# Optimization experiments

Hardware: AMD Instinct MI355X
Metric: run time of the kernel (lower is better)

Reference implementation:

```python
import jax, jax.numpy as jnp
import numpy as np

N_QUBITS = 4
N_LAYERS = 3
SHORT_W = 2048
LONG_W = 8192
BATCH = 2048


def _conv1d(x, w, b, pad):
    # x: [B, Cin, L], w: [Cout, Cin, K]
    y = jax.lax.conv_general_dilated(x, w, window_strides=(1,), padding=[(pad, pad)],
                                     dimension_numbers=("NCH", "OIH", "NCH"))
    return y + b[None, :, None]


def _ry_mat(t):
    c, s = jnp.cos(t / 2), jnp.sin(t / 2)
    return jnp.stack([jnp.stack([c, -s]), jnp.stack([s, c])]).astype(jnp.complex64)


def _rz_mat(a):
    return jnp.diag(jnp.stack([jnp.exp(-0.5j * a), jnp.exp(0.5j * a)])).astype(jnp.complex64)


def _rot_mat(phi, theta, omega):
    # PennyLane Rot(phi, theta, omega) = RZ(omega) @ RY(theta) @ RZ(phi)
    return _rz_mat(omega) @ _ry_mat(theta) @ _rz_mat(phi)


def _apply_1q(state, U, wire):
    state = jnp.tensordot(U, state, axes=((1,), (wire,)))
    return jnp.moveaxis(state, 0, wire)


def _apply_cnot(state, c, t):
    s0 = jax.lax.index_in_dim(state, 0, axis=c, keepdims=True)
    s1 = jax.lax.index_in_dim(state, 1, axis=c, keepdims=True)
    s1 = jnp.flip(s1, axis=t)
    return jnp.concatenate([s0, s1], axis=c)


def _circuit(x, w):
    # x: [4] real features, w: [3, 4, 3] StronglyEntanglingLayers weights
    state = jnp.zeros((2,) * N_QUBITS, jnp.complex64).at[(0,) * N_QUBITS].set(1.0)
    for i in range(N_QUBITS):
        state = _apply_1q(state, _ry_mat(jnp.pi * x[i]), i)
    for l in range(N_LAYERS):
        r = (l % (N_QUBITS - 1)) + 1  # default PennyLane ranges: 1,2,3
        for i in range(N_QUBITS):
            state = _apply_1q(state, _rot_mat(w[l, i, 0], w[l, i, 1], w[l, i, 2]), i)
        for i in range(N_QUBITS):
            state = _apply_cnot(state, i, (i + r) % N_QUBITS)
    probs = jnp.abs(state) ** 2
    zs = []
    for i in range(N_QUBITS):
        p = probs.sum(axis=tuple(a for a in range(N_QUBITS) if a != i))
        zs.append(p[0] - p[1])  # <PauliZ_i>
    return jnp.stack(zs)


def setup_inputs() -> dict:
    key = jax.random.key(0)
    ks = jax.random.split(key, 13)
    d = {}
    d["xs"] = jax.random.normal(ks[0], (BATCH, 1, SHORT_W), jnp.float32)
    d["xl"] = jax.random.normal(ks[1], (BATCH, 1, LONG_W), jnp.float32)
    d["cs_conv_w"] = jax.random.normal(ks[2], (8, 1, 3), jnp.float32) * 0.3
    d["cs_conv_b"] = jax.random.normal(ks[3], (8,), jnp.float32) * 0.1
    d["cs_lin_w"] = jax.random.normal(ks[4], (2, 8 * SHORT_W), jnp.float32) * (1.0 / np.sqrt(8 * SHORT_W))
    d["cs_lin_b"] = jax.random.normal(ks[5], (2,), jnp.float32) * 0.1
    d["cl_conv_w"] = jax.random.normal(ks[6], (8, 1, 5), jnp.float32) * 0.3
    d["cl_conv_b"] = jax.random.normal(ks[7], (8,), jnp.float32) * 0.1
    d["cl_lin_w"] = jax.random.normal(ks[8], (2, 8 * LONG_W // 2), jnp.float32) * (1.0 / np.sqrt(8 * LONG_W // 2))
    d["cl_lin_b"] = jax.random.normal(ks[9], (2,), jnp.float32) * 0.1
    d["rw"] = jax.random.normal(ks[10], (N_LAYERS, N_QUBITS, 3), jnp.float32)
    d["fc_w"] = jax.random.normal(ks[11], (1, N_QUBITS), jnp.float32) * 0.5
    d["fc_b"] = jax.random.normal(ks[12], (1,), jnp.float32) * 0.1
    return d


def reference(xs, xl, cs_conv_w, cs_conv_b, cs_lin_w, cs_lin_b,
              cl_conv_w, cl_conv_b, cl_lin_w, cl_lin_b, rw, fc_w, fc_b):
    B = xs.shape[0]
    # short branch: conv(k=3,p=1) -> relu -> flatten -> linear
    hs = jax.nn.relu(_conv1d(xs, cs_conv_w, cs_conv_b, 1)).reshape(B, -1)
    fs = hs @ cs_lin_w.T + cs_lin_b  # [B, 2]
    # long branch: conv(k=5,p=2) -> relu -> maxpool(2) -> flatten -> linear
    hl = jax.nn.relu(_conv1d(xl, cl_conv_w, cl_conv_b, 2))
    hl = hl.reshape(B, 8, LONG_W // 2, 2).max(axis=-1).reshape(B, -1)
    fl = hl @ cl_lin_w.T + cl_lin_b  # [B, 2]
    f = jnp.concatenate([fs, fl], axis=1)  # [B, 4]
    # original detaches features before the quantum circuit
    f = jax.lax.stop_gradient(f)
    rw_c = jax.lax.stop_gradient(rw)
    qo = jax.vmap(lambda x: _circuit(x, rw_c))(f).astype(jnp.float32)  # [B, 4]
    return qo @ fc_w.T + fc_b  # [B, 1]
```

## Files before the change

### kernel.cpp

```cpp
#include <hip/hip_runtime.h>
#include <math.h>

namespace {
constexpr int kB  = 2048;
constexpr int kSW = 2048;
constexpr int kLW = 8192;
constexpr int kLP = kLW / 2;
constexpr int kROWS = 4;
constexpr int kLBLKS = (kB / kROWS) * 2;
constexpr int kSBLKS = (kB / kROWS) * 2;
}

__device__ __forceinline__ void long_half(
    int blk, int h, const float* __restrict__ xl, const float* __restrict__ cw,
    const float* __restrict__ cb, const float* __restrict__ lw,
    float* __restrict__ part) {
  __shared__ float red[kROWS][2][4];
  const int tid = threadIdx.x;
  const int b0 = blk * kROWS;

  float wgt[8][5], bias[8];
#pragma unroll
  for (int c = 0; c < 8; ++c) {
#pragma unroll
    for (int k = 0; k < 5; ++k) wgt[c][k] = cw[c * 5 + k];
    bias[c] = cb[c];
  }

  float acc[kROWS][2];
#pragma unroll
  for (int r = 0; r < kROWS; ++r) { acc[r][0] = 0.f; acc[r][1] = 0.f; }

  for (int ch = 0; ch < 2; ++ch) {
    const int p0 = h * 2048 + ch * 1024 + tid * 4;
    const int s  = 2 * p0;

    float w[kROWS][12];
#pragma unroll
    for (int r = 0; r < kROWS; ++r) {
      const float* x = xl + (size_t)(b0 + r) * kLW;
      float2 hm = (p0 > 0) ? *reinterpret_cast<const float2*>(x + s - 2)
                           : make_float2(0.f, 0.f);
      float4 f0 = *reinterpret_cast<const float4*>(x + s);
      float4 f1 = *reinterpret_cast<const float4*>(x + s + 4);
      float2 f2 = (s + 8 < kLW) ? *reinterpret_cast<const float2*>(x + s + 8)
                                : make_float2(0.f, 0.f);
      w[r][0] = hm.x; w[r][1] = hm.y;
      w[r][2] = f0.x; w[r][3] = f0.y; w[r][4] = f0.z; w[r][5] = f0.w;
      w[r][6] = f1.x; w[r][7] = f1.y; w[r][8] = f1.z; w[r][9] = f1.w;
      w[r][10] = f2.x; w[r][11] = f2.y;
    }
    float4 la4[8], lb4[8];
#pragma unroll
    for (int c = 0; c < 8; ++c) {
      la4[c] = *reinterpret_cast<const float4*>(lw + (size_t)c * kLP + p0);
      lb4[c] = *reinterpret_cast<const float4*>(lw + (size_t)(8 + c) * kLP + p0);
    }

#pragma unroll
    for (int c = 0; c < 8; ++c) {
      const float la[4] = {la4[c].x, la4[c].y, la4[c].z, la4[c].w};
      const float lbv[4] = {lb4[c].x, lb4[c].y, lb4[c].z, lb4[c].w};
#pragma unroll
      for (int r = 0; r < kROWS; ++r) {
#pragma unroll
        for (int u = 0; u < 4; ++u) {
          float v0 = fmaf(wgt[c][0], w[r][2 * u + 0],
                     fmaf(wgt[c][1], w[r][2 * u + 1],
                     fmaf(wgt[c][2], w[r][2 * u + 2],
                     fmaf(wgt[c][3], w[r][2 * u + 3],
                     fmaf(wgt[c][4], w[r][2 * u + 4], bias[c])))));
          float v1 = fmaf(wgt[c][0], w[r][2 * u + 1],
                     fmaf(wgt[c][1], w[r][2 * u + 2],
                     fmaf(wgt[c][2], w[r][2 * u + 3],
                     fmaf(wgt[c][3], w[r][2 * u + 4],
                     fmaf(wgt[c][4], w[r][2 * u + 5], bias[c])))));
          const float m = fmaxf(fmaxf(v0, v1), 0.f);
          acc[r][0] = fmaf(m, la[u], acc[r][0]);
          acc[r][1] = fmaf(m, lbv[u], acc[r][1]);
        }
      }
    }
  }

#pragma unroll
  for (int r = 0; r < kROWS; ++r)
#pragma unroll
    for (int o = 0; o < 2; ++o) {
      float a = acc[r][o];
#pragma unroll
      for (int off = 32; off > 0; off >>= 1) a += __shfl_down(a, off);
      if ((tid & 63) == 0) red[r][o][tid >> 6] = a;
    }
  __syncthreads();
  if (tid < kROWS * 2) {
    const int r = tid >> 1, o = tid & 1;
    part[(size_t)h * kB * 4 + (size_t)(b0 + r) * 4 + 2 + o] =
        red[r][o][0] + red[r][o][1] + red[r][o][2] + red[r][o][3];
  }
}

__device__ __forceinline__ void short_half(
    int blk, int h, const float* __restrict__ xs, const float* __restrict__ cw,
    const float* __restrict__ cb, const float* __restrict__ lw,
    float* __restrict__ part) {
  __shared__ float red[kROWS][2][4];
  const int tid = threadIdx.x;
  const int b0 = blk * kROWS;

  float wgt[8][3], bias[8];
#pragma unroll
  for (int c = 0; c < 8; ++c) {
#pragma unroll
    for (int k = 0; k < 3; ++k) wgt[c][k] = cw[c * 3 + k];
    bias[c] = cb[c];
  }

  float acc[kROWS][2];
#pragma unroll
  for (int r = 0; r < kROWS; ++r) { acc[r][0] = 0.f; acc[r][1] = 0.f; }

  {
    const int p0 = h * 1024 + tid * 4;

    float w[kROWS][6];
#pragma unroll
    for (int r = 0; r < kROWS; ++r) {
      const float* x = xs + (size_t)(b0 + r) * kSW;
      float xm = (p0 > 0) ? x[p0 - 1] : 0.f;
      float4 f0 = *reinterpret_cast<const float4*>(x + p0);
      float xp = (p0 + 4 < kSW) ? x[p0 + 4] : 0.f;
      w[r][0] = xm;
      w[r][1] = f0.x; w[r][2] = f0.y; w[r][3] = f0.z; w[r][4] = f0.w;
      w[r][5] = xp;
    }
    float4 la4[8], lb4[8];
#pragma unroll
    for (int c = 0; c < 8; ++c) {
      la4[c] = *reinterpret_cast<const float4*>(lw + (size_t)c * kSW + p0);
      lb4[c] = *reinterpret_cast<const float4*>(lw + (size_t)(8 + c) * kSW + p0);
    }

#pragma unroll
    for (int c = 0; c < 8; ++c) {
      const float la[4] = {la4[c].x, la4[c].y, la4[c].z, la4[c].w};
      const float lbv[4] = {lb4[c].x, lb4[c].y, lb4[c].z, lb4[c].w};
#pragma unroll
      for (int r = 0; r < kROWS; ++r) {
#pragma unroll
        for (int u = 0; u < 4; ++u) {
          float v = fmaf(wgt[c][0], w[r][u],
                    fmaf(wgt[c][1], w[r][u + 1],
                    fmaf(wgt[c][2], w[r][u + 2], bias[c])));
          const float m = fmaxf(v, 0.f);
          acc[r][0] = fmaf(m, la[u], acc[r][0]);
          acc[r][1] = fmaf(m, lbv[u], acc[r][1]);
        }
      }
    }
  }

#pragma unroll
  for (int r = 0; r < kROWS; ++r)
#pragma unroll
    for (int o = 0; o < 2; ++o) {
      float a = acc[r][o];
#pragma unroll
      for (int off = 32; off > 0; off >>= 1) a += __shfl_down(a, off);
      if ((tid & 63) == 0) red[r][o][tid >> 6] = a;
    }
  __syncthreads();
  if (tid < kROWS * 2) {
    const int r = tid >> 1, o = tid & 1;
    part[(size_t)h * kB * 4 + (size_t)(b0 + r) * 4 + o] =
        red[r][o][0] + red[r][o][1] + red[r][o][2] + red[r][o][3];
  }
}

__global__ __launch_bounds__(256, 3) void features_kernel(
    const float* __restrict__ xs, const float* __restrict__ cs_cw,
    const float* __restrict__ cs_cb, const float* __restrict__ cs_lw,
    const float* __restrict__ xl, const float* __restrict__ cl_cw,
    const float* __restrict__ cl_cb, const float* __restrict__ cl_lw,
    float* __restrict__ part) {
  const int bid = blockIdx.x;
  if (bid < kLBLKS)
    long_half(bid >> 1, bid & 1, xl, cl_cw, cl_cb, cl_lw, part);
  else {
    const int s = bid - kLBLKS;
    short_half(s >> 1, s & 1, xs, cs_cw, cs_cb, cs_lw, part);
  }
}

template <int MASK>
__device__ __forceinline__ void apply_1q(float (&ar)[16], float (&ai)[16],
                                         float u00r, float u00i, float u01r, float u01i,
                                         float u10r, float u10i, float u11r, float u11i) {
#pragma unroll
  for (int i = 0; i < 16; ++i) {
    if (!(i & MASK)) {
      const int j = i | MASK;
      const float a0r = ar[i], a0i = ai[i];
      const float a1r = ar[j], a1i = ai[j];
      ar[i] = u00r * a0r - u00i * a0i + u01r * a1r - u01i * a1i;
      ai[i] = u00r * a0i + u00i * a0r + u01r * a1i + u01i * a1r;
      ar[j] = u10r * a0r - u10i * a0i + u11r * a1r - u11i * a1i;
      ai[j] = u10r * a0i + u10i * a0r + u11r * a1i + u11i * a1r;
    }
  }
}

template <int MASK>
__device__ __forceinline__ void apply_ry(float (&ar)[16], float (&ai)[16], float half_t) {
  float s, c;
  sincosf(half_t, &s, &c);
  apply_1q<MASK>(ar, ai, c, 0.f, -s, 0.f, s, 0.f, c, 0.f);
}

template <int MASK>
__device__ __forceinline__ void apply_rot(float (&ar)[16], float (&ai)[16],
                                          float phi, float theta, float omega) {
  float st, ct; sincosf(0.5f * theta, &st, &ct);
  float sa, ca; sincosf(0.5f * (phi + omega), &sa, &ca);
  float sm, cm; sincosf(0.5f * (phi - omega), &sm, &cm);
  apply_1q<MASK>(ar, ai,
                 ct * ca, -ct * sa,
                 -st * cm, -st * sm,
                 st * cm, -st * sm,
                 ct * ca, ct * sa);
}

template <int MC, int MT>
__device__ __forceinline__ void apply_cnot(float (&ar)[16], float (&ai)[16]) {
#pragma unroll
  for (int i = 0; i < 16; ++i) {
    if ((i & MC) && !(i & MT)) {
      const int j = i | MT;
      float t;
      t = ar[i]; ar[i] = ar[j]; ar[j] = t;
      t = ai[i]; ai[i] = ai[j]; ai[j] = t;
    }
  }
}

__global__ __launch_bounds__(64) void quantum_kernel(
    const float* __restrict__ part, const float* __restrict__ cs_lb,
    const float* __restrict__ cl_lb, const float* __restrict__ rw,
    const float* __restrict__ fcw, const float* __restrict__ fcb,
    float* __restrict__ out) {
  const int b = blockIdx.x * 64 + threadIdx.x;
  if (b >= kB) return;

  const float f0 = part[(size_t)b * 4 + 0] + part[(size_t)kB * 4 + b * 4 + 0] + cs_lb[0];
  const float f1 = part[(size_t)b * 4 + 1] + part[(size_t)kB * 4 + b * 4 + 1] + cs_lb[1];
  const float f2 = part[(size_t)b * 4 + 2] + part[(size_t)kB * 4 + b * 4 + 2] + cl_lb[0];
  const float f3 = part[(size_t)b * 4 + 3] + part[(size_t)kB * 4 + b * 4 + 3] + cl_lb[1];

  float ar[16], ai[16];
#pragma unroll
  for (int i = 0; i < 16; ++i) { ar[i] = 0.f; ai[i] = 0.f; }
  ar[0] = 1.f;

  const float kHalfPi = 1.57079632679489662f;
  apply_ry<8>(ar, ai, kHalfPi * f0);
  apply_ry<4>(ar, ai, kHalfPi * f1);
  apply_ry<2>(ar, ai, kHalfPi * f2);
  apply_ry<1>(ar, ai, kHalfPi * f3);

  apply_rot<8>(ar, ai, rw[0], rw[1], rw[2]);
  apply_rot<4>(ar, ai, rw[3], rw[4], rw[5]);
  apply_rot<2>(ar, ai, rw[6], rw[7], rw[8]);
  apply_rot<1>(ar, ai, rw[9], rw[10], rw[11]);
  apply_cnot<8, 4>(ar, ai);
  apply_cnot<4, 2>(ar, ai);
  apply_cnot<2, 1>(ar, ai);
  apply_cnot<1, 8>(ar, ai);

  apply_rot<8>(ar, ai, rw[12], rw[13], rw[14]);
  apply_rot<4>(ar, ai, rw[15], rw[16], rw[17]);
  apply_rot<2>(ar, ai, rw[18], rw[19], rw[20]);
  apply_rot<1>(ar, ai, rw[21], rw[22], rw[23]);
  apply_cnot<8, 2>(ar, ai);
  apply_cnot<4, 1>(ar, ai);
  apply_cnot<2, 8>(ar, ai);
  apply_cnot<1, 4>(ar, ai);

  apply_rot<8>(ar, ai, rw[24], rw[25], rw[26]);
  apply_rot<4>(ar, ai, rw[27], rw[28], rw[29]);
  apply_rot<2>(ar, ai, rw[30], rw[31], rw[32]);
  apply_rot<1>(ar, ai, rw[33], rw[34], rw[35]);
  apply_cnot<8, 1>(ar, ai);
  apply_cnot<4, 8>(ar, ai);
  apply_cnot<2, 4>(ar, ai);
  apply_cnot<1, 2>(ar, ai);

  float z0 = 0.f, z1 = 0.f, z2 = 0.f, z3 = 0.f;
#pragma unroll
  for (int i = 0; i < 16; ++i) {
    const float p = ar[i] * ar[i] + ai[i] * ai[i];
    z0 += (i & 8) ? -p : p;
    z1 += (i & 4) ? -p : p;
    z2 += (i & 2) ? -p : p;
    z3 += (i & 1) ? -p : p;
  }
  out[b] = fcb[0] + z0 * fcw[0] + z1 * fcw[1] + z2 * fcw[2] + z3 * fcw[3];
}

extern "C" void kernel_launch(void* const* d_in, const int* in_sizes, int n_in,
                              void* d_out, int out_size, void* d_ws, size_t ws_size,
                              hipStream_t stream) {
  const float* xs     = (const float*)d_in[0];
  const float* xl     = (const float*)d_in[1];
  const float* cs_cw  = (const float*)d_in[2];
  const float* cs_cb  = (const float*)d_in[3];
  const float* cs_lw  = (const float*)d_in[4];
  const float* cs_lb  = (const float*)d_in[5];
  const float* cl_cw  = (const float*)d_in[6];
  const float* cl_cb  = (const float*)d_in[7];
  const float* cl_lw  = (const float*)d_in[8];
  const float* cl_lb  = (const float*)d_in[9];
  const float* rw     = (const float*)d_in[10];
  const float* fcw    = (const float*)d_in[11];
  const float* fcb    = (const float*)d_in[12];
  float* out  = (float*)d_out;
  float* part = (float*)d_ws;

  hipLaunchKernelGGL(features_kernel, dim3(kLBLKS + kSBLKS), dim3(256), 0, stream,
                     xs, cs_cw, cs_cb, cs_lw,
                     xl, cl_cw, cl_cb, cl_lw, part);
  hipLaunchKernelGGL(quantum_kernel, dim3(kB / 64), dim3(64), 0, stream,
                     part, cs_lb, cl_lb, rw, fcw, fcb, out);
}
```

Before: 46.52 us.

## Split long-branch work into quarters, interleave block types, pin operands in registers

Each long-branch block now covers one quarter of the pooled sequence instead of a half with an inner two-chunk loop. Long and short blocks are interleaved two-to-one in the grid so both kinds are spread evenly across CUs. Linear-weight and input values are loaded once up front and pinned in VGPRs with empty asm, and rows are processed in pairs to keep register pressure down. The partial-sum layout changes to separate short and long buffers, with the quantum kernel summing four long partials. This means more blocks and more partial writes, and the register pinning may hurt occupancy or scheduling.

```diff
diff --git a/kernel.cpp b/kernel.cpp
--- a/kernel.cpp
+++ b/kernel.cpp
@@ -7,14 +7,15 @@
 constexpr int kLW = 8192;
 constexpr int kLP = kLW / 2;
 constexpr int kROWS = 4;
-constexpr int kLBLKS = (kB / kROWS) * 2;
-constexpr int kSBLKS = (kB / kROWS) * 2;
-}
-
-__device__ __forceinline__ void long_half(
-    int blk, int h, const float* __restrict__ xl, const float* __restrict__ cw,
+constexpr int kNBLK = 3072;
+}
+
+__device__ __forceinline__ void pin(float& x) { asm volatile("" : "+v"(x)); }
+
+__device__ __forceinline__ void long_quarter(
+    int blk, int q, const float* __restrict__ xl, const float* __restrict__ cw,
     const float* __restrict__ cb, const float* __restrict__ lw,
-    float* __restrict__ part) {
+    float* __restrict__ partL) {
   __shared__ float red[kROWS][2][4];
   const int tid = threadIdx.x;
   const int b0 = blk * kROWS;
@@ -27,18 +28,32 @@
     bias[c] = cb[c];
   }
 
+  const int p0 = q * 1024 + tid * 4;
+  const int s  = 2 * p0;
+
+  float la[8][4], lbv[8][4];
+#pragma unroll
+  for (int c = 0; c < 8; ++c) {
+    float4 a4 = *reinterpret_cast<const float4*>(lw + (size_t)c * kLP + p0);
+    float4 b4 = *reinterpret_cast<const float4*>(lw + (size_t)(8 + c) * kLP + p0);
+    la[c][0] = a4.x; la[c][1] = a4.y; la[c][2] = a4.z; la[c][3] = a4.w;
+    lbv[c][0] = b4.x; lbv[c][1] = b4.y; lbv[c][2] = b4.z; lbv[c][3] = b4.w;
+  }
+#pragma unroll
+  for (int c = 0; c < 8; ++c)
+#pragma unroll
+    for (int u = 0; u < 4; ++u) { pin(la[c][u]); pin(lbv[c][u]); }
+
   float acc[kROWS][2];
 #pragma unroll
   for (int r = 0; r < kROWS; ++r) { acc[r][0] = 0.f; acc[r][1] = 0.f; }
 
-  for (int ch = 0; ch < 2; ++ch) {
-    const int p0 = h * 2048 + ch * 1024 + tid * 4;
-    const int s  = 2 * p0;
-
-    float w[kROWS][12];
-#pragma unroll
-    for (int r = 0; r < kROWS; ++r) {
-      const float* x = xl + (size_t)(b0 + r) * kLW;
+#pragma unroll
+  for (int g = 0; g < 2; ++g) {
+    float w[2][12];
+#pragma unroll
+    for (int r = 0; r < 2; ++r) {
+      const float* x = xl + (size_t)(b0 + g * 2 + r) * kLW;
       float2 hm = (p0 > 0) ? *reinterpret_cast<const float2*>(x + s - 2)
                            : make_float2(0.f, 0.f);
       float4 f0 = *reinterpret_cast<const float4*>(x + s);
@@ -50,19 +65,16 @@
       w[r][6] = f1.x; w[r][7] = f1.y; w[r][8] = f1.z; w[r][9] = f1.w;
       w[r][10] = f2.x; w[r][11] = f2.y;
     }
-    float4 la4[8], lb4[8];
+#pragma unroll
+    for (int r = 0; r < 2; ++r)
+#pragma unroll
+      for (int k = 0; k < 12; ++k) pin(w[r][k]);
+
 #pragma unroll
     for (int c = 0; c < 8; ++c) {
-      la4[c] = *reinterpret_cast<const float4*>(lw + (size_t)c * kLP + p0);
-      lb4[c] = *reinterpret_cast<const float4*>(lw + (size_t)(8 + c) * kLP + p0);
-    }
-
-#pragma unroll
-    for (int c = 0; c < 8; ++c) {
-      const float la[4] = {la4[c].x, la4[c].y, la4[c].z, la4[c].w};
-      const float lbv[4] = {lb4[c].x, lb4[c].y, lb4[c].z, lb4[c].w};
-#pragma unroll
-      for (int r = 0; r < kROWS; ++r) {
+#pragma unroll
+      for (int r = 0; r < 2; ++r) {
+        const int rr = g * 2 + r;
 #pragma unroll
         for (int u = 0; u < 4; ++u) {
           float v0 = fmaf(wgt[c][0], w[r][2 * u + 0],
@@ -76,8 +88,8 @@
                      fmaf(wgt[c][3], w[r][2 * u + 4],
                      fmaf(wgt[c][4], w[r][2 * u + 5], bias[c])))));
           const float m = fmaxf(fmaxf(v0, v1), 0.f);
-          acc[r][0] = fmaf(m, la[u], acc[r][0]);
-          acc[r][1] = fmaf(m, lbv[u], acc[r][1]);
+          acc[rr][0] = fmaf(m, la[c][u], acc[rr][0]);
+          acc[rr][1] = fmaf(m, lbv[c][u], acc[rr][1]);
         }
       }
     }
@@ -95,7 +107,7 @@
   __syncthreads();
   if (tid < kROWS * 2) {
     const int r = tid >> 1, o = tid & 1;
-    part[(size_t)h * kB * 4 + (size_t)(b0 + r) * 4 + 2 + o] =
+    partL[(size_t)q * kB * 2 + (size_t)(b0 + r) * 2 + o] =
         red[r][o][0] + red[r][o][1] + red[r][o][2] + red[r][o][3];
   }
 }
@@ -103,7 +115,7 @@
 __device__ __forceinline__ void short_half(
     int blk, int h, const float* __restrict__ xs, const float* __restrict__ cw,
     const float* __restrict__ cb, const float* __restrict__ lw,
-    float* __restrict__ part) {
+    float* __restrict__ partS) {
   __shared__ float red[kROWS][2][4];
   const int tid = threadIdx.x;
   const int b0 = blk * kROWS;
@@ -116,46 +128,53 @@
     bias[c] = cb[c];
   }
 
+  const int p0 = h * 1024 + tid * 4;
+
+  float la[8][4], lbv[8][4];
+#pragma unroll
+  for (int c = 0; c < 8; ++c) {
+    float4 a4 = *reinterpret_cast<const float4*>(lw + (size_t)c * kSW + p0);
+    float4 b4 = *reinterpret_cast<const float4*>(lw + (size_t)(8 + c) * kSW + p0);
+    la[c][0] = a4.x; la[c][1] = a4.y; la[c][2] = a4.z; la[c][3] = a4.w;
+    lbv[c][0] = b4.x; lbv[c][1] = b4.y; lbv[c][2] = b4.z; lbv[c][3] = b4.w;
+  }
+#pragma unroll
+  for (int c = 0; c < 8; ++c)
+#pragma unroll
+    for (int u = 0; u < 4; ++u) { pin(la[c][u]); pin(lbv[c][u]); }
+
+  float w[kROWS][6];
+#pragma unroll
+  for (int r = 0; r < kROWS; ++r) {
+    const float* x = xs + (size_t)(b0 + r) * kSW;
+    float xm = (p0 > 0) ? x[p0 - 1] : 0.f;
+    float4 f0 = *reinterpret_cast<const float4*>(x + p0);
+    float xp = (p0 + 4 < kSW) ? x[p0 + 4] : 0.f;
+    w[r][0] = xm;
+    w[r][1] = f0.x; w[r][2] = f0.y; w[r][3] = f0.z; w[r][4] = f0.w;
+    w[r][5] = xp;
+  }
+#pragma unroll
+  for (int r = 0; r < kROWS; ++r)
+#pragma unroll
+    for (int k = 0; k < 6; ++k) pin(w[r][k]);
+
   float acc[kROWS][2];
 #pragma unroll
   for (int r = 0; r < kROWS; ++r) { acc[r][0] = 0.f; acc[r][1] = 0.f; }
 
-  {
-    const int p0 = h * 1024 + tid * 4;
-
-    float w[kROWS][6];
+#pragma unroll
+  for (int c = 0; c < 8; ++c) {
 #pragma unroll
     for (int r = 0; r < kROWS; ++r) {
-      const float* x = xs + (size_t)(b0 + r) * kSW;
-      float xm = (p0 > 0) ? x[p0 - 1] : 0.f;
-      float4 f0 = *reinterpret_cast<const float4*>(x + p0);
-      float xp = (p0 + 4 < kSW) ? x[p0 + 4] : 0.f;
-      w[r][0] = xm;
-      w[r][1] = f0.x; w[r][2] = f0.y; w[r][3] = f0.z; w[r][4] = f0.w;
-      w[r][5] = xp;
-    }
-    float4 la4[8], lb4[8];
-#pragma unroll
-    for (int c = 0; c < 8; ++c) {
-      la4[c] = *reinterpret_cast<const float4*>(lw + (size_t)c * kSW + p0);
-      lb4[c] = *reinterpret_cast<const float4*>(lw + (size_t)(8 + c) * kSW + p0);
-    }
-
-#pragma unroll
-    for (int c = 0; c < 8; ++c) {
-      const float la[4] = {la4[c].x, la4[c].y, la4[c].z, la4[c].w};
-      const float lbv[4] = {lb4[c].x, lb4[c].y, lb4[c].z, lb4[c].w};
-#pragma unroll
-      for (int r = 0; r < kROWS; ++r) {
-#pragma unroll
-        for (int u = 0; u < 4; ++u) {
-          float v = fmaf(wgt[c][0], w[r][u],
-                    fmaf(wgt[c][1], w[r][u + 1],
-                    fmaf(wgt[c][2], w[r][u + 2], bias[c])));
-          const float m = fmaxf(v, 0.f);
-          acc[r][0] = fmaf(m, la[u], acc[r][0]);
-          acc[r][1] = fmaf(m, lbv[u], acc[r][1]);
-        }
+#pragma unroll
+      for (int u = 0; u < 4; ++u) {
+        float v = fmaf(wgt[c][0], w[r][u],
+                  fmaf(wgt[c][1], w[r][u + 1],
+                  fmaf(wgt[c][2], w[r][u + 2], bias[c])));
+        const float m = fmaxf(v, 0.f);
+        acc[r][0] = fmaf(m, la[c][u], acc[r][0]);
+        acc[r][1] = fmaf(m, lbv[c][u], acc[r][1]);
       }
     }
   }
@@ -172,7 +191,7 @@
   __syncthreads();
   if (tid < kROWS * 2) {
     const int r = tid >> 1, o = tid & 1;
-    part[(size_t)h * kB * 4 + (size_t)(b0 + r) * 4 + o] =
+    partS[(size_t)h * kB * 2 + (size_t)(b0 + r) * 2 + o] =
         red[r][o][0] + red[r][o][1] + red[r][o][2] + red[r][o][3];
   }
 }
@@ -182,13 +201,15 @@
     const float* __restrict__ cs_cb, const float* __restrict__ cs_lw,
     const float* __restrict__ xl, const float* __restrict__ cl_cw,
     const float* __restrict__ cl_cb, const float* __restrict__ cl_lw,
-    float* __restrict__ part) {
+    float* __restrict__ partS, float* __restrict__ partL) {
   const int bid = blockIdx.x;
-  if (bid < kLBLKS)
-    long_half(bid >> 1, bid & 1, xl, cl_cw, cl_cb, cl_lw, part);
-  else {
-    const int s = bid - kLBLKS;
-    short_half(s >> 1, s & 1, xs, cs_cw, cs_cb, cs_lw, part);
+  const int tri = bid / 3, rem = bid % 3;
+  if (rem < 2) {
+    const int li = tri * 2 + rem;
+    long_quarter(li >> 2, li & 3, xl, cl_cw, cl_cb, cl_lw, partL);
+  } else {
+    const int si = tri;
+    short_half(si >> 1, si & 1, xs, cs_cw, cs_cb, cs_lw, partS);
   }
 }
 
@@ -244,17 +265,21 @@
 }
 
 __global__ __launch_bounds__(64) void quantum_kernel(
-    const float* __restrict__ part, const float* __restrict__ cs_lb,
-    const float* __restrict__ cl_lb, const float* __restrict__ rw,
-    const float* __restrict__ fcw, const float* __restrict__ fcb,
-    float* __restrict__ out) {
+    const float* __restrict__ partS, const float* __restrict__ partL,
+    const float* __restrict__ cs_lb, const float* __restrict__ cl_lb,
+    const float* __restrict__ rw, const float* __restrict__ fcw,
+    const float* __restrict__ fcb, float* __restrict__ out) {
   const int b = blockIdx.x * 64 + threadIdx.x;
   if (b >= kB) return;
 
-  const float f0 = part[(size_t)b * 4 + 0] + part[(size_t)kB * 4 + b * 4 + 0] + cs_lb[0];
-  const float f1 = part[(size_t)b * 4 + 1] + part[(size_t)kB * 4 + b * 4 + 1] + cs_lb[1];
-  const float f2 = part[(size_t)b * 4 + 2] + part[(size_t)kB * 4 + b * 4 + 2] + cl_lb[0];
-  const float f3 = part[(size_t)b * 4 + 3] + part[(size_t)kB * 4 + b * 4 + 3] + cl_lb[1];
+  const float f0 = partS[(size_t)b * 2 + 0] + partS[(size_t)kB * 2 + b * 2 + 0] + cs_lb[0];
+  const float f1 = partS[(size_t)b * 2 + 1] + partS[(size_t)kB * 2 + b * 2 + 1] + cs_lb[1];
+  float f2 = cl_lb[0], f3 = cl_lb[1];
+#pragma unroll
+  for (int q = 0; q < 4; ++q) {
+    f2 += partL[(size_t)q * kB * 2 + b * 2 + 0];
+    f3 += partL[(size_t)q * kB * 2 + b * 2 + 1];
+  }
 
   float ar[16], ai[16];
 #pragma unroll
@@ -322,12 +347,13 @@
   const float* rw     = (const float*)d_in[10];
   const float* fcw    = (const float*)d_in[11];
   const float* fcb    = (const float*)d_in[12];
-  float* out  = (float*)d_out;
-  float* part = (float*)d_ws;
-
-  hipLaunchKernelGGL(features_kernel, dim3(kLBLKS + kSBLKS), dim3(256), 0, stream,
+  float* out   = (float*)d_out;
+  float* partS = (float*)d_ws;
+  float* partL = (float*)d_ws + 2 * kB * 2;
+
+  hipLaunchKernelGGL(features_kernel, dim3(kNBLK), dim3(256), 0, stream,
                      xs, cs_cw, cs_cb, cs_lw,
-                     xl, cl_cw, cl_cb, cl_lw, part);
+                     xl, cl_cw, cl_cb, cl_lw, partS, partL);
   hipLaunchKernelGGL(quantum_kernel, dim3(kB / 64), dim3(64), 0, stream,
-                     part, cs_lb, cl_lb, rw, fcw, fcb, out);
-}
+                     partS, partL, cs_lb, cl_lb, rw, fcw, fcb, out);
+}
```

After: 54.84 us. 17.9% more time.
